# Kernel tuning notes

Hardware: AMD Instinct MI355X
Metric: run time of the kernel (lower is better)

The kernel has to match this reference:

```python
import jax, jax.numpy as jnp
import numpy as np

N_NODES = 100000
N_EDGES = 1600000
GENE_DIM = 256
HID = 128
NUM_CLASSES = 2
BN_EPS = 1e-5


def setup_inputs() -> dict:
    key = jax.random.key(0)
    ks = jax.random.split(key, 24)
    g = lambda k, shape, scale: (jax.random.normal(k, shape, dtype=jnp.float32) * scale)
    inp = {
        "x": g(ks[0], (N_NODES, GENE_DIM), 1.0),
        "edge_index": jax.random.randint(ks[1], (2, N_EDGES), 0, N_NODES, dtype=jnp.int64),
        # GCNConv weights (glorot-ish scale) and biases
        "W1": g(ks[2], (GENE_DIM, HID), 1.0 / np.sqrt(GENE_DIM)), "b1": jnp.zeros((HID,), jnp.float32),
        "W2": g(ks[3], (HID, 2 * HID), 1.0 / np.sqrt(HID)), "b2": jnp.zeros((2 * HID,), jnp.float32),
        "W3": g(ks[4], (2 * HID, HID), 1.0 / np.sqrt(2 * HID)), "b3": jnp.zeros((HID,), jnp.float32),
        "W4": g(ks[5], (HID, HID // 2), 1.0 / np.sqrt(HID)), "b4": jnp.zeros((HID // 2,), jnp.float32),
        "Wc": g(ks[6], (HID // 2, NUM_CLASSES), 1.0 / np.sqrt(HID // 2)), "bc": jnp.zeros((NUM_CLASSES,), jnp.float32),
        # BatchNorm affine params
        "g1": jnp.ones((HID,), jnp.float32), "be1": jnp.zeros((HID,), jnp.float32),
        "g2": jnp.ones((2 * HID,), jnp.float32), "be2": jnp.zeros((2 * HID,), jnp.float32),
        "g3": jnp.ones((HID,), jnp.float32), "be3": jnp.zeros((HID,), jnp.float32),
        "g4": jnp.ones((HID // 2,), jnp.float32), "be4": jnp.zeros((HID // 2,), jnp.float32),
    }
    return inp


def _batchnorm(h, gamma, beta):
    # training-mode BatchNorm1d: per-feature batch stats (biased variance)
    mean = h.mean(axis=0)
    var = ((h - mean) ** 2).mean(axis=0)
    return gamma * (h - mean) * jax.lax.rsqrt(var + BN_EPS) + beta


def _gcn_conv(h, W, b, src, dst, norm, n):
    # PyG GCNConv: linear transform, then sym-normalized aggregation over
    # edges (self-loops already included in src/dst/norm), then bias.
    m = h @ W                                   # [n, d_out]
    msg = m[src] * norm[:, None]                # [E+n, d_out] gather
    agg = jax.ops.segment_sum(msg, dst, num_segments=n)  # scatter-add
    return agg + b


def reference(x, edge_index, W1, b1, W2, b2, W3, b3, W4, b4, Wc, bc,
              g1, be1, g2, be2, g3, be3, g4, be4):
    n = x.shape[0]
    loop = jnp.arange(n, dtype=edge_index.dtype)
    src = jnp.concatenate([edge_index[0], loop])  # add self-loops
    dst = jnp.concatenate([edge_index[1], loop])
    deg = jax.ops.segment_sum(jnp.ones_like(dst, dtype=x.dtype), dst, num_segments=n)
    dinv = jax.lax.rsqrt(jnp.maximum(deg, 1.0))
    norm = dinv[src] * dinv[dst]                  # D^-1/2 (A+I) D^-1/2

    h = jax.nn.relu(_gcn_conv(x, W1, b1, src, dst, norm, n))
    h = _batchnorm(h, g1, be1)
    h = jax.nn.relu(_gcn_conv(h, W2, b2, src, dst, norm, n))
    h = _batchnorm(h, g2, be2)
    h = jax.nn.relu(_gcn_conv(h, W3, b3, src, dst, norm, n))
    h = _batchnorm(h, g3, be3)
    out4 = jax.nn.relu(_gcn_conv(h, W4, b4, src, dst, norm, n))
    bn4 = _batchnorm(out4, g4, be4)
    logits = bn4 @ Wc + bc
    return (logits, out4, bn4)
```

## Files before the change

### kernel.cpp

```cpp
#include <hip/hip_runtime.h>
#include <hip/hip_bf16.h>

#define N_NODES 100000
#define N_EDGES 1600000
#define NB ((N_NODES + 255) / 256)
#define CHUNK 16384
#define NBLK ((N_EDGES + CHUNK - 1) / CHUNK)
#define NSHADOW 64

typedef short sh8 __attribute__((ext_vector_type(8)));
typedef float f32x4 __attribute__((ext_vector_type(4)));

__device__ __forceinline__ float bf2f(unsigned short s) {
    return __uint_as_float(((unsigned int)s) << 16);
}
__device__ __forceinline__ unsigned short f2bf(float f) {
    unsigned int u = __float_as_uint(f);
    unsigned int r = (u + 0x7FFFu + ((u >> 16) & 1u)) >> 16;
    return (unsigned short)r;
}
__device__ __forceinline__ float blo(unsigned int u) { return __uint_as_float(u << 16); }
__device__ __forceinline__ float bhi(unsigned int u) { return __uint_as_float(u & 0xffff0000u); }


__global__ __launch_bounds__(256) void k_hist(const int* __restrict__ ei, int* __restrict__ histG) {
    __shared__ int hist[NB];
    int blk = blockIdx.x, t = threadIdx.x;
    for (int b = t; b < NB; b += 256) hist[b] = 0;
    __syncthreads();
    int e0 = blk * CHUNK;
    int e1 = min(e0 + CHUNK, N_EDGES);
    for (int e = e0 + t; e < e1; e += 256) atomicAdd(&hist[ei[N_EDGES + e] >> 8], 1);
    __syncthreads();
    for (int b = t; b < NB; b += 256) histG[b * NBLK + blk] = hist[b];
}

__global__ __launch_bounds__(128) void k_scanrow(int* __restrict__ histG, int* __restrict__ rowsum) {
    __shared__ int sm[128];
    int b = blockIdx.x, t = threadIdx.x;
    int v = (t < NBLK) ? histG[b * NBLK + t] : 0;
    sm[t] = v; __syncthreads();
    for (int d = 1; d < 128; d <<= 1) {
        int add = (t >= d) ? sm[t - d] : 0;
        __syncthreads(); sm[t] += add; __syncthreads();
    }
    if (t < NBLK) histG[b * NBLK + t] = sm[t] - v;
    if (t == 127) rowsum[b] = sm[127];
}

__global__ __launch_bounds__(512) void k_scanbkt(const int* __restrict__ rowsum, int* __restrict__ rowbase) {
    __shared__ int sm[512];
    int t = threadIdx.x;
    int v = (t < NB) ? rowsum[t] : 0;
    sm[t] = v; __syncthreads();
    for (int d = 1; d < 512; d <<= 1) {
        int add = (t >= d) ? sm[t - d] : 0;
        __syncthreads(); sm[t] += add; __syncthreads();
    }
    if (t <= NB) rowbase[t] = sm[t] - v;
}

__global__ __launch_bounds__(256) void k_part(const int* __restrict__ ei, const int* __restrict__ histG,
                                              const int* __restrict__ rowbase, unsigned* __restrict__ pairs) {
    __shared__ int cur[NB];
    int blk = blockIdx.x, t = threadIdx.x;
    for (int b = t; b < NB; b += 256) cur[b] = rowbase[b] + histG[b * NBLK + blk];
    __syncthreads();
    int e0 = blk * CHUNK;
    int e1 = min(e0 + CHUNK, N_EDGES);
    for (int e = e0 + t; e < e1; e += 256) {
        int s = ei[e], d = ei[N_EDGES + e];
        int pos = atomicAdd(&cur[d >> 8], 1);
        pairs[pos] = ((unsigned)s << 8) | (unsigned)(d & 255);
    }
}

__global__ __launch_bounds__(256) void k_bsort(const unsigned* __restrict__ pairs, const int* __restrict__ rowbase,
                                               int* __restrict__ col, int* __restrict__ basep,
                                               int* __restrict__ deg, float* __restrict__ dinv,
                                               float* __restrict__ sdeg) {
    __shared__ int cnt[256];
    __shared__ int sm[256];
    __shared__ int cur[256];
    int b = blockIdx.x, t = threadIdx.x;
    int base = rowbase[b], end = rowbase[b + 1];
    cnt[t] = 0; __syncthreads();
    for (int e = base + t; e < end; e += 256) atomicAdd(&cnt[pairs[e] & 255], 1);
    __syncthreads();
    int v = cnt[t];
    sm[t] = v; __syncthreads();
    for (int d = 1; d < 256; d <<= 1) {
        int add = (t >= d) ? sm[t - d] : 0;
        __syncthreads(); sm[t] += add; __syncthreads();
    }
    int excl = sm[t] - v;
    cur[t] = excl;
    int gd = (b << 8) + t;
    if (gd < N_NODES) {
        basep[gd] = base + excl;
        deg[gd] = v;
        dinv[gd] = rsqrtf((float)(v + 1));
        sdeg[gd] = sqrtf((float)(v + 1));
    }
    __syncthreads();
    for (int e = base + t; e < end; e += 256) {
        unsigned p = pairs[e];
        int pos = atomicAdd(&cur[p & 255], 1);
        col[base + pos] = (int)(p >> 8);
    }
}

__global__ __launch_bounds__(256) void k_svec(const int* __restrict__ col, const int* __restrict__ basep,
                                              const int* __restrict__ deg, const float* __restrict__ dinv,
                                              float* __restrict__ svec) {
    int w = (blockIdx.x * 256 + threadIdx.x) >> 6;
    if (w >= N_NODES) return;
    int lane = threadIdx.x & 63;
    int start = basep[w], cnt = deg[w];
    float s = 0.f;
    for (int j = lane; j < cnt; j += 64) s += dinv[col[start + j]];
#pragma unroll
    for (int off = 32; off; off >>= 1) s += __shfl_down(s, off, 64);
    if (lane == 0) { float di = dinv[w]; svec[w] = di * (s + di); }
}


__global__ void k_wconv_all(const float* __restrict__ W1, const float* __restrict__ W2,
                            const float* __restrict__ W3, const float* __restrict__ W4,
                            unsigned short* __restrict__ Wt1, unsigned short* __restrict__ Wt2,
                            unsigned short* __restrict__ Wt3, unsigned short* __restrict__ Wt4) {
    int idx = blockIdx.x * 256 + threadIdx.x;
    const float* W; unsigned short* Wt; int K, N, base;
    if (idx < 32768)       { W = W1; Wt = Wt1; K = 256; N = 128; base = 0; }
    else if (idx < 65536)  { W = W2; Wt = Wt2; K = 128; N = 256; base = 32768; }
    else if (idx < 98304)  { W = W3; Wt = Wt3; K = 256; N = 128; base = 65536; }
    else if (idx < 106496) { W = W4; Wt = Wt4; K = 128; N = 64;  base = 98304; }
    else return;
    int li = idx - base;
    int n = li / K, k = li - n * K;
    Wt[li] = f2bf(W[(size_t)k * N + n]);
}


__global__ __launch_bounds__(256) void k_bnred(float* __restrict__ shadow, float* __restrict__ dst) {
    int f = blockIdx.x * 256 + threadIdx.x;
    float s = 0.f;
#pragma unroll
    for (int i = 0; i < NSHADOW; ++i) {
        s += shadow[i * 512 + f];
        shadow[i * 512 + f] = 0.f;
    }
    dst[f] = s;
}


template <int D, bool INF32, bool RESCALE>
__global__ __launch_bounds__(256) void k_bnstats(const void* __restrict__ h,
                                                 const float* __restrict__ sdeg,
                                                 float* __restrict__ shadow) {
    constexpr int VEC = INF32 ? 4 : 8;
    constexpr int TPR = D / VEC;
    constexpr int RPB = 256 / TPR;
    const int tid = threadIdx.x;
    const int rg = tid / TPR;
    const int oc = tid % TPR;
    const int fb = oc * VEC;

    float s1[VEC], s2[VEC];
#pragma unroll
    for (int k = 0; k < VEC; ++k) { s1[k] = 0.f; s2[k] = 0.f; }

    for (int r = blockIdx.x * RPB + rg; r < N_NODES; r += gridDim.x * RPB) {
        float rs = 1.f;
        if constexpr (RESCALE) rs = sdeg[r];
        if constexpr (INF32) {
            float4 v = *(const float4*)((const float*)h + (size_t)r * D + fb);
            float vv[4] = {v.x, v.y, v.z, v.w};
#pragma unroll
            for (int k = 0; k < 4; ++k) {
                float val = vv[k];
                if constexpr (RESCALE) val *= rs;
                s1[k] += val; s2[k] += val * val;
            }
        } else {
            uint4 u = *(const uint4*)((const unsigned short*)h + (size_t)r * D + fb);
            unsigned uu[4] = {u.x, u.y, u.z, u.w};
#pragma unroll
            for (int k = 0; k < 4; ++k) {
                float v0 = blo(uu[k]), v1 = bhi(uu[k]);
                if constexpr (RESCALE) { v0 *= rs; v1 *= rs; }
                s1[2 * k] += v0;     s2[2 * k] += v0 * v0;
                s1[2 * k + 1] += v1; s2[2 * k + 1] += v1 * v1;
            }
        }
    }

    __shared__ float red[2][D];
    for (int i = tid; i < 2 * D; i += 256) ((float*)red)[i] = 0.f;
    __syncthreads();
#pragma unroll
    for (int k = 0; k < VEC; ++k) {
        atomicAdd(&red[0][fb + k], s1[k]);
        atomicAdd(&red[1][fb + k], s2[k]);
    }
    __syncthreads();
    float* slot = shadow + ((blockIdx.x & (NSHADOW - 1)) << 9);
    for (int i = tid; i < 2 * D; i += 256) {
        int f = (i < D) ? i : (256 + i - D);
        float v = (i < D) ? red[0][i] : red[1][i - D];
        atomicAdd(&slot[f], v);
    }
}


template <int BN, int NWM, int NWN, int AMODE, bool BIASRELU, bool DSCALE, bool STATS>
__global__ __launch_bounds__(256) void k_gemm_bf(const void* __restrict__ Ain,
                                                 const unsigned short* __restrict__ Wt,
                                                 const float* __restrict__ sums_in,
                                                 const float* __restrict__ gamma,
                                                 const float* __restrict__ beta,
                                                 const float* __restrict__ svec,
                                                 const float* __restrict__ bias,
                                                 const float* __restrict__ dinv,
                                                 unsigned short* __restrict__ Mout,
                                                 float* __restrict__ sums_out,
                                                 int K, int NTOT) {
    constexpr int BK = 64;
    constexpr int LDA = BK + 8;
    constexpr int MF = 128 / (16 * NWM);
    constexpr int NF = BN / (16 * NWN);
    __shared__ unsigned short As[128 * LDA];
    __shared__ unsigned short Bs[BN * LDA];
    __shared__ float ss_sc[256];
    __shared__ float ss_sh[256];
    const int tid = threadIdx.x;
    const int lane = tid & 63;
    const int w = tid >> 6;
    const int wm = w / NWN, wn = w % NWN;
    const int row0 = blockIdx.x * 128;
    const int col0 = blockIdx.y * BN;

    if constexpr (AMODE >= 1) {
        for (int f = tid; f < K; f += 256) {
            float mean = sums_in[f] * (1.f / N_NODES);
            float var = sums_in[256 + f] * (1.f / N_NODES) - mean * mean;
            float inv = rsqrtf(var + 1e-5f);
            float sc = gamma[f] * inv;
            ss_sc[f] = sc;
            ss_sh[f] = beta[f] - mean * sc;
        }
        __syncthreads();
    }

    f32x4 acc[MF][NF];
#pragma unroll
    for (int i = 0; i < MF; ++i)
#pragma unroll
        for (int j = 0; j < NF; ++j)
#pragma unroll
            for (int r = 0; r < 4; ++r) acc[i][j][r] = 0.f;

    const int sr = tid >> 3;
    const int scc = (tid & 7) * 8;

    for (int k0 = 0; k0 < K; k0 += BK) {
#pragma unroll
        for (int p = 0; p < 4; ++p) {
            int r = p * 32 + sr;
            int gr = row0 + r;
            alignas(16) unsigned short tmp[8];
            if constexpr (AMODE == 0) {
                const float* Af = (const float*)Ain;
                float4 v0 = make_float4(0.f, 0.f, 0.f, 0.f), v1 = v0;
                if (gr < N_NODES) {
                    const float* p0 = Af + (size_t)gr * K + k0 + scc;
                    v0 = *(const float4*)p0;
                    v1 = *(const float4*)(p0 + 4);
                }
                tmp[0] = f2bf(v0.x); tmp[1] = f2bf(v0.y); tmp[2] = f2bf(v0.z); tmp[3] = f2bf(v0.w);
                tmp[4] = f2bf(v1.x); tmp[5] = f2bf(v1.y); tmp[6] = f2bf(v1.z); tmp[7] = f2bf(v1.w);
            } else {
                const unsigned short* Ab = (const unsigned short*)Ain;
                uint4 raw = make_uint4(0, 0, 0, 0);
                if (gr < N_NODES) raw = *(const uint4*)(Ab + (size_t)gr * K + k0 + scc);
                const unsigned short* pr = (const unsigned short*)&raw;
                float sv = 1.f;
                if constexpr (AMODE == 2) sv = (gr < N_NODES) ? svec[gr] : 0.f;
#pragma unroll
                for (int q = 0; q < 8; ++q) {
                    float sc = ss_sc[k0 + scc + q];
                    float sh = ss_sh[k0 + scc + q];
                    float val;
                    if constexpr (AMODE == 2) val = bf2f(pr[q]) * sc + sh * sv;
                    else val = bf2f(pr[q]) * sc + sh;
                    tmp[q] = f2bf(val);
                }
            }
            *(uint4*)&As[r * LDA + scc] = *(const uint4*)tmp;
        }
        constexpr int BP = (BN * BK) / 2048;
#pragma unroll
        for (int p = 0; p < BP; ++p) {
            int r = p * 32 + sr;
            uint4 raw = *(const uint4*)(Wt + (size_t)(col0 + r) * K + k0 + scc);
            *(uint4*)&Bs[r * LDA + scc] = raw;
        }
        __syncthreads();
#pragma unroll
        for (int ks = 0; ks < 2; ++ks) {
            sh8 af[MF], bfr[NF];
#pragma unroll
            for (int i = 0; i < MF; ++i)
                af[i] = *(const sh8*)&As[(wm * MF * 16 + i * 16 + (lane & 15)) * LDA + ks * 32 + (lane >> 4) * 8];
#pragma unroll
            for (int j = 0; j < NF; ++j)
                bfr[j] = *(const sh8*)&Bs[(wn * NF * 16 + j * 16 + (lane & 15)) * LDA + ks * 32 + (lane >> 4) * 8];
#pragma unroll
            for (int i = 0; i < MF; ++i)
#pragma unroll
                for (int j = 0; j < NF; ++j)
                    acc[i][j] = __builtin_amdgcn_mfma_f32_16x16x32_bf16(af[i], bfr[j], acc[i][j], 0, 0, 0);
        }
        __syncthreads();
    }

    float cs[NF], cs2[NF];
    if constexpr (STATS) {
#pragma unroll
        for (int j = 0; j < NF; ++j) { cs[j] = 0.f; cs2[j] = 0.f; }
    }
#pragma unroll
    for (int i = 0; i < MF; ++i) {
#pragma unroll
        for (int r = 0; r < 4; ++r) {
            int grow = row0 + wm * MF * 16 + i * 16 + (lane >> 4) * 4 + r;
            if (grow >= N_NODES) continue;
            float rsc = 1.f;
            if constexpr (DSCALE) rsc = dinv[grow];
#pragma unroll
            for (int j = 0; j < NF; ++j) {
                int gcol = col0 + wn * NF * 16 + j * 16 + (lane & 15);
                float v = acc[i][j][r];
                if constexpr (BIASRELU) v = fmaxf(v + bias[gcol], 0.f);
                if constexpr (DSCALE) v *= rsc;
                if constexpr (STATS) { cs[j] += v; cs2[j] += v * v; }
                Mout[(size_t)grow * NTOT + gcol] = f2bf(v);
            }
        }
    }
    if constexpr (STATS) {
        __shared__ float red[2][BN];
        for (int i = tid; i < 2 * BN; i += 256) ((float*)red)[i] = 0.f;
        __syncthreads();
#pragma unroll
        for (int j = 0; j < NF; ++j) {
            int lc = wn * NF * 16 + j * 16 + (lane & 15);
            atomicAdd(&red[0][lc], cs[j]);
            atomicAdd(&red[1][lc], cs2[j]);
        }
        __syncthreads();
        for (int f = tid; f < BN; f += 256) {
            atomicAdd(&sums_out[col0 + f], red[0][f]);
            atomicAdd(&sums_out[256 + col0 + f], red[1][f]);
        }
    }
}


template <int D, bool PRE, bool OUTF32, bool OUTSCALE>
__global__ __launch_bounds__(256) void k_agg(const unsigned short* __restrict__ m,
                                             const int* __restrict__ col,
                                             const int* __restrict__ basep,
                                             const int* __restrict__ deg,
                                             const float* __restrict__ dinv,
                                             const float* __restrict__ bias,
                                             void* __restrict__ out) {
    constexpr int VPL = D / 64;
    const int w = (blockIdx.x * 256 + threadIdx.x) >> 6;
    if (w >= N_NODES) return;
    const int lane = threadIdx.x & 63;
    const int fo = lane * VPL;
    const unsigned short* mfo = m + fo;
    float acc[VPL];
#pragma unroll
    for (int k = 0; k < VPL; ++k) acc[k] = 0.f;

    int start = basep[w], cnt = deg[w];
    int j = 0;
    for (; j + 8 <= cnt; j += 8) {
        int sx[8];
#pragma unroll
        for (int i = 0; i < 8; ++i) sx[i] = col[start + j + i];
        if constexpr (VPL == 2) {
            unsigned u[8];
#pragma unroll
            for (int i = 0; i < 8; ++i) u[i] = *(const unsigned*)(mfo + (size_t)sx[i] * D);
#pragma unroll
            for (int i = 0; i < 8; ++i) { acc[0] += blo(u[i]); acc[1] += bhi(u[i]); }
        } else {
            float v[8];
#pragma unroll
            for (int i = 0; i < 8; ++i) v[i] = bf2f(mfo[(size_t)sx[i] * D]);
#pragma unroll
            for (int i = 0; i < 8; ++i) acc[0] += v[i];
        }
    }
    for (; j < cnt; ++j) {
        int s0 = col[start + j];
        if constexpr (VPL == 2) {
            unsigned u0 = *(const unsigned*)(mfo + (size_t)s0 * D);
            acc[0] += blo(u0); acc[1] += bhi(u0);
        } else {
            acc[0] += bf2f(mfo[(size_t)s0 * D]);
        }
    }
    if constexpr (VPL == 2) {
        unsigned u0 = *(const unsigned*)(mfo + (size_t)w * D);
        acc[0] += blo(u0); acc[1] += bhi(u0);
    } else {
        acc[0] += bf2f(mfo[(size_t)w * D]);
    }

    float di = dinv[w];
    float o[VPL];
    if constexpr (PRE) {
#pragma unroll
        for (int k = 0; k < VPL; ++k) o[k] = acc[k] * di;
    } else {
#pragma unroll
        for (int k = 0; k < VPL; ++k) {
            o[k] = fmaxf(acc[k] * di + bias[fo + k], 0.f);
            if constexpr (OUTSCALE) o[k] *= di;
        }
    }

    if constexpr (OUTF32) {
        float* of = (float*)out;
#pragma unroll
        for (int k = 0; k < VPL; ++k) of[(size_t)w * D + fo + k] = o[k];
    } else {
        unsigned short* ob = (unsigned short*)out + (size_t)w * D + fo;
        if constexpr (VPL == 2) {
            unsigned int u = (unsigned)f2bf(o[0]) | ((unsigned)f2bf(o[1]) << 16);
            *(unsigned int*)ob = u;
        } else {
            ob[0] = f2bf(o[0]);
        }
    }
}


__global__ __launch_bounds__(256) void k_bnlog(const float* __restrict__ out4, const float* __restrict__ sums,
                                               const float* __restrict__ gamma, const float* __restrict__ beta,
                                               const float* __restrict__ Wc, const float* __restrict__ bc,
                                               float* __restrict__ bn4, float* __restrict__ logits) {
    int gw = (blockIdx.x * 256 + threadIdx.x) >> 6;
    if (gw >= N_NODES) return;
    int f = threadIdx.x & 63;
    float mean = sums[f] * (1.f / N_NODES);
    float var = sums[256 + f] * (1.f / N_NODES) - mean * mean;
    float inv = rsqrtf(var + 1e-5f);
    float sc = gamma[f] * inv;
    float sh = beta[f] - mean * sc;
    float v = out4[(size_t)gw * 64 + f];
    float bn = v * sc + sh;
    bn4[(size_t)gw * 64 + f] = bn;
    float a0 = bn * Wc[2 * f];
    float a1 = bn * Wc[2 * f + 1];
#pragma unroll
    for (int off = 32; off; off >>= 1) {
        a0 += __shfl_down(a0, off, 64);
        a1 += __shfl_down(a1, off, 64);
    }
    if (f == 0) {
        logits[2 * gw] = a0 + bc[0];
        logits[2 * gw + 1] = a1 + bc[1];
    }
}


extern "C" void kernel_launch(void* const* d_in, const int* in_sizes, int n_in,
                              void* d_out, int out_size, void* d_ws, size_t ws_size,
                              hipStream_t stream) {
    const float* x  = (const float*)d_in[0];
    const int* ei   = (const int*)d_in[1];
    const float* W1 = (const float*)d_in[2];  const float* b1  = (const float*)d_in[3];
    const float* W2 = (const float*)d_in[4];  const float* b2  = (const float*)d_in[5];
    const float* W3 = (const float*)d_in[6];  const float* b3  = (const float*)d_in[7];
    const float* W4 = (const float*)d_in[8];  const float* b4  = (const float*)d_in[9];
    const float* Wc = (const float*)d_in[10]; const float* bc  = (const float*)d_in[11];
    const float* g1 = (const float*)d_in[12]; const float* be1 = (const float*)d_in[13];
    const float* g2 = (const float*)d_in[14]; const float* be2 = (const float*)d_in[15];
    const float* g3 = (const float*)d_in[16]; const float* be3 = (const float*)d_in[17];
    const float* g4 = (const float*)d_in[18]; const float* be4 = (const float*)d_in[19];

    char* wsb = (char*)d_ws;
    size_t off = 0;
    auto alloc = [&](size_t bytes) -> void* {
        void* p = wsb + off;
        off = (off + bytes + 511) & ~(size_t)511;
        return p;
    };
    int* deg     = (int*)alloc((size_t)N_NODES * 4);
    int* basep   = (int*)alloc((size_t)N_NODES * 4);
    float* dinv  = (float*)alloc((size_t)N_NODES * 4);
    float* sdeg  = (float*)alloc((size_t)N_NODES * 4);
    float* svec  = (float*)alloc((size_t)N_NODES * 4);
    int* col     = (int*)alloc((size_t)N_EDGES * 4);
    unsigned* pairs = (unsigned*)alloc((size_t)N_EDGES * 4);
    int* histG   = (int*)alloc((size_t)NB * NBLK * 4);
    int* rowsum  = (int*)alloc((size_t)NB * 4);
    int* rowbase = (int*)alloc((size_t)(NB + 1) * 4);
    float* sums  = (float*)alloc(2048 * 4);
    float* shadow = (float*)alloc((size_t)NSHADOW * 512 * 4);
    unsigned short* Wt1 = (unsigned short*)alloc((size_t)256 * 128 * 2);
    unsigned short* Wt2 = (unsigned short*)alloc((size_t)128 * 256 * 2);
    unsigned short* Wt3 = (unsigned short*)alloc((size_t)256 * 128 * 2);
    unsigned short* Wt4 = (unsigned short*)alloc((size_t)128 * 64 * 2);
    unsigned short* mb = (unsigned short*)alloc((size_t)N_NODES * 128 * 2);
    unsigned short* hb = (unsigned short*)alloc((size_t)N_NODES * 256 * 2);

    float* sums1 = sums, *sums2 = sums + 512, *sums3 = sums + 1024, *sums4 = sums + 1536;

    float* outLogits = (float*)d_out;
    float* out4 = outLogits + (size_t)N_NODES * 2;
    float* bn4  = out4 + (size_t)N_NODES * 64;

    hipMemsetAsync(sums, 0, 2048 * 4, stream);
    hipMemsetAsync(shadow, 0, (size_t)NSHADOW * 512 * 4, stream);

    k_hist<<<NBLK, 256, 0, stream>>>(ei, histG);
    k_scanrow<<<NB, 128, 0, stream>>>(histG, rowsum);
    k_scanbkt<<<1, 512, 0, stream>>>(rowsum, rowbase);
    k_part<<<NBLK, 256, 0, stream>>>(ei, histG, rowbase, pairs);
    k_bsort<<<NB, 256, 0, stream>>>(pairs, rowbase, col, basep, deg, dinv, sdeg);
    k_svec<<<(N_NODES + 3) / 4, 256, 0, stream>>>(col, basep, deg, dinv, svec);

    k_wconv_all<<<(106496 + 255) / 256, 256, 0, stream>>>(W1, W2, W3, W4, Wt1, Wt2, Wt3, Wt4);

    const int GBM = (N_NODES + 127) / 128;
    const int AB = (N_NODES + 3) / 4;
    const int SB = 512;

    k_gemm_bf<128, 2, 2, 0, false, true, false><<<dim3(GBM, 1), 256, 0, stream>>>(
        x, Wt1, nullptr, nullptr, nullptr, nullptr, nullptr, dinv, mb, nullptr, 256, 128);
    k_agg<128, false, false, true><<<AB, 256, 0, stream>>>(
        mb, col, basep, deg, dinv, b1, hb);
    k_bnstats<128, false, true><<<SB, 256, 0, stream>>>(hb, sdeg, shadow);
    k_bnred<<<2, 256, 0, stream>>>(shadow, sums1);

    k_agg<128, true, false, false><<<AB, 256, 0, stream>>>(
        hb, col, basep, deg, dinv, nullptr, mb);
    k_gemm_bf<128, 2, 2, 2, true, false, true><<<dim3(GBM, 2), 256, 0, stream>>>(
        mb, Wt2, sums1, g1, be1, svec, b2, nullptr, hb, sums2, 128, 256);

    k_gemm_bf<128, 2, 2, 1, false, true, false><<<dim3(GBM, 1), 256, 0, stream>>>(
        hb, Wt3, sums2, g2, be2, nullptr, nullptr, dinv, mb, nullptr, 256, 128);
    k_agg<128, false, false, false><<<AB, 256, 0, stream>>>(
        mb, col, basep, deg, dinv, b3, hb);
    k_bnstats<128, false, false><<<SB, 256, 0, stream>>>(hb, nullptr, shadow);
    k_bnred<<<2, 256, 0, stream>>>(shadow, sums3);

    k_gemm_bf<64, 4, 1, 1, false, true, false><<<dim3(GBM, 1), 256, 0, stream>>>(
        hb, Wt4, sums3, g3, be3, nullptr, nullptr, dinv, mb, nullptr, 128, 64);
    k_agg<64, false, true, false><<<AB, 256, 0, stream>>>(
        mb, col, basep, deg, dinv, b4, out4);
    k_bnstats<64, true, false><<<SB, 256, 0, stream>>>(out4, nullptr, shadow);
    k_bnred<<<2, 256, 0, stream>>>(shadow, sums4);
    k_bnlog<<<(N_NODES * 64 + 255) / 256, 256, 0, stream>>>(out4, sums4, g4, be4, Wc, bc, bn4, outLogits);
}
```

Before: 629.6 us.

## Register-prefetch GEMM tiles, halve row tile, move layer-2 BN stats to separate kernel

Replaces the bf16 MFMA GEMM with a version that loads the next K-tile from global memory into registers while the current tile is being multiplied, then writes it to LDS afterwards. The row tile drops from 128 to 64 to launch more blocks, and the warp layouts change. BatchNorm statistics are no longer fused into the layer-2 GEMM epilogue; a separate k_bnstats/k_bnred pass over the 256-wide output computes them instead. That extra pass adds a full read of the activation, and the prefetch registers add register pressure.

```diff
diff --git a/kernel.cpp b/kernel.cpp
--- a/kernel.cpp
+++ b/kernel.cpp
@@ -213,23 +213,23 @@
 }
 
 
-template <int BN, int NWM, int NWN, int AMODE, bool BIASRELU, bool DSCALE, bool STATS>
-__global__ __launch_bounds__(256) void k_gemm_bf(const void* __restrict__ Ain,
-                                                 const unsigned short* __restrict__ Wt,
-                                                 const float* __restrict__ sums_in,
-                                                 const float* __restrict__ gamma,
-                                                 const float* __restrict__ beta,
-                                                 const float* __restrict__ svec,
-                                                 const float* __restrict__ bias,
-                                                 const float* __restrict__ dinv,
-                                                 unsigned short* __restrict__ Mout,
-                                                 float* __restrict__ sums_out,
-                                                 int K, int NTOT) {
+template <int BN, int NWM, int NWN, int AMODE, bool BIASRELU, bool DSCALE>
+__global__ __launch_bounds__(256) void k_gemm2(const void* __restrict__ Ain,
+                                               const unsigned short* __restrict__ Wt,
+                                               const float* __restrict__ sums_in,
+                                               const float* __restrict__ gamma,
+                                               const float* __restrict__ beta,
+                                               const float* __restrict__ svec,
+                                               const float* __restrict__ bias,
+                                               const float* __restrict__ dinv,
+                                               unsigned short* __restrict__ Mout,
+                                               int K, int NTOT) {
     constexpr int BK = 64;
-    constexpr int LDA = BK + 8;
-    constexpr int MF = 128 / (16 * NWM);
+    constexpr int LDA = 72;
+    constexpr int MF = 64 / (16 * NWM);
     constexpr int NF = BN / (16 * NWN);
-    __shared__ unsigned short As[128 * LDA];
+    constexpr int BP = BN / 32;
+    __shared__ unsigned short As[64 * LDA];
     __shared__ unsigned short Bs[BN * LDA];
     __shared__ float ss_sc[256];
     __shared__ float ss_sh[256];
@@ -237,7 +237,7 @@
     const int lane = tid & 63;
     const int w = tid >> 6;
     const int wm = w / NWN, wn = w % NWN;
-    const int row0 = blockIdx.x * 128;
+    const int row0 = blockIdx.x * 64;
     const int col0 = blockIdx.y * BN;
 
     if constexpr (AMODE >= 1) {
@@ -252,60 +252,85 @@
         __syncthreads();
     }
 
-    f32x4 acc[MF][NF];
-#pragma unroll
-    for (int i = 0; i < MF; ++i)
-#pragma unroll
-        for (int j = 0; j < NF; ++j)
-#pragma unroll
-            for (int r = 0; r < 4; ++r) acc[i][j][r] = 0.f;
-
     const int sr = tid >> 3;
     const int scc = (tid & 7) * 8;
 
-    for (int k0 = 0; k0 < K; k0 += BK) {
-#pragma unroll
-        for (int p = 0; p < 4; ++p) {
+    float4 fa[2][2];
+    uint4 ua[2];
+    uint4 ub[BP];
+    float sv[2];
+
+    auto LOAD = [&](int k0) {
+        if constexpr (AMODE == 0) {
+            const float* Af = (const float*)Ain;
+#pragma unroll
+            for (int p = 0; p < 2; ++p) {
+                int gr = row0 + p * 32 + sr;
+                fa[p][0] = make_float4(0.f, 0.f, 0.f, 0.f); fa[p][1] = fa[p][0];
+                if (gr < N_NODES) {
+                    const float* p0 = Af + (size_t)gr * K + k0 + scc;
+                    fa[p][0] = *(const float4*)p0;
+                    fa[p][1] = *(const float4*)(p0 + 4);
+                }
+            }
+        } else {
+            const unsigned short* Ab = (const unsigned short*)Ain;
+#pragma unroll
+            for (int p = 0; p < 2; ++p) {
+                int gr = row0 + p * 32 + sr;
+                ua[p] = make_uint4(0, 0, 0, 0);
+                if (gr < N_NODES) ua[p] = *(const uint4*)(Ab + (size_t)gr * K + k0 + scc);
+                if constexpr (AMODE == 2) sv[p] = (gr < N_NODES) ? svec[gr] : 0.f;
+            }
+        }
+#pragma unroll
+        for (int p = 0; p < BP; ++p) {
             int r = p * 32 + sr;
-            int gr = row0 + r;
+            ub[p] = *(const uint4*)(Wt + (size_t)(col0 + r) * K + k0 + scc);
+        }
+    };
+
+    auto WRITE = [&](int k0) {
+#pragma unroll
+        for (int p = 0; p < 2; ++p) {
             alignas(16) unsigned short tmp[8];
             if constexpr (AMODE == 0) {
-                const float* Af = (const float*)Ain;
-                float4 v0 = make_float4(0.f, 0.f, 0.f, 0.f), v1 = v0;
-                if (gr < N_NODES) {
-                    const float* p0 = Af + (size_t)gr * K + k0 + scc;
-                    v0 = *(const float4*)p0;
-                    v1 = *(const float4*)(p0 + 4);
-                }
-                tmp[0] = f2bf(v0.x); tmp[1] = f2bf(v0.y); tmp[2] = f2bf(v0.z); tmp[3] = f2bf(v0.w);
-                tmp[4] = f2bf(v1.x); tmp[5] = f2bf(v1.y); tmp[6] = f2bf(v1.z); tmp[7] = f2bf(v1.w);
+                tmp[0] = f2bf(fa[p][0].x); tmp[1] = f2bf(fa[p][0].y);
+                tmp[2] = f2bf(fa[p][0].z); tmp[3] = f2bf(fa[p][0].w);
+                tmp[4] = f2bf(fa[p][1].x); tmp[5] = f2bf(fa[p][1].y);
+                tmp[6] = f2bf(fa[p][1].z); tmp[7] = f2bf(fa[p][1].w);
             } else {
-                const unsigned short* Ab = (const unsigned short*)Ain;
-                uint4 raw = make_uint4(0, 0, 0, 0);
-                if (gr < N_NODES) raw = *(const uint4*)(Ab + (size_t)gr * K + k0 + scc);
-                const unsigned short* pr = (const unsigned short*)&raw;
-                float sv = 1.f;
-                if constexpr (AMODE == 2) sv = (gr < N_NODES) ? svec[gr] : 0.f;
+                const unsigned short* pr = (const unsigned short*)&ua[p];
 #pragma unroll
                 for (int q = 0; q < 8; ++q) {
                     float sc = ss_sc[k0 + scc + q];
                     float sh = ss_sh[k0 + scc + q];
                     float val;
-                    if constexpr (AMODE == 2) val = bf2f(pr[q]) * sc + sh * sv;
+                    if constexpr (AMODE == 2) val = bf2f(pr[q]) * sc + sh * sv[p];
                     else val = bf2f(pr[q]) * sc + sh;
                     tmp[q] = f2bf(val);
                 }
             }
-            *(uint4*)&As[r * LDA + scc] = *(const uint4*)tmp;
-        }
-        constexpr int BP = (BN * BK) / 2048;
-#pragma unroll
-        for (int p = 0; p < BP; ++p) {
-            int r = p * 32 + sr;
-            uint4 raw = *(const uint4*)(Wt + (size_t)(col0 + r) * K + k0 + scc);
-            *(uint4*)&Bs[r * LDA + scc] = raw;
-        }
-        __syncthreads();
+            *(uint4*)&As[(p * 32 + sr) * LDA + scc] = *(const uint4*)tmp;
+        }
+#pragma unroll
+        for (int p = 0; p < BP; ++p) *(uint4*)&Bs[(p * 32 + sr) * LDA + scc] = ub[p];
+    };
+
+    f32x4 acc[MF][NF];
+#pragma unroll
+    for (int i = 0; i < MF; ++i)
+#pragma unroll
+        for (int j = 0; j < NF; ++j)
+#pragma unroll
+            for (int r = 0; r < 4; ++r) acc[i][j][r] = 0.f;
+
+    LOAD(0);
+    WRITE(0);
+    __syncthreads();
+    const int nk = K / BK;
+    for (int kt = 1; kt <= nk; ++kt) {
+        if (kt < nk) LOAD(kt * BK);
 #pragma unroll
         for (int ks = 0; ks < 2; ++ks) {
             sh8 af[MF], bfr[NF];
@@ -322,13 +347,12 @@
                     acc[i][j] = __builtin_amdgcn_mfma_f32_16x16x32_bf16(af[i], bfr[j], acc[i][j], 0, 0, 0);
         }
         __syncthreads();
-    }
-
-    float cs[NF], cs2[NF];
-    if constexpr (STATS) {
-#pragma unroll
-        for (int j = 0; j < NF; ++j) { cs[j] = 0.f; cs2[j] = 0.f; }
-    }
+        if (kt < nk) {
+            WRITE(kt * BK);
+            __syncthreads();
+        }
+    }
+
 #pragma unroll
     for (int i = 0; i < MF; ++i) {
 #pragma unroll
@@ -343,25 +367,8 @@
                 float v = acc[i][j][r];
                 if constexpr (BIASRELU) v = fmaxf(v + bias[gcol], 0.f);
                 if constexpr (DSCALE) v *= rsc;
-                if constexpr (STATS) { cs[j] += v; cs2[j] += v * v; }
                 Mout[(size_t)grow * NTOT + gcol] = f2bf(v);
             }
-        }
-    }
-    if constexpr (STATS) {
-        __shared__ float red[2][BN];
-        for (int i = tid; i < 2 * BN; i += 256) ((float*)red)[i] = 0.f;
-        __syncthreads();
-#pragma unroll
-        for (int j = 0; j < NF; ++j) {
-            int lc = wn * NF * 16 + j * 16 + (lane & 15);
-            atomicAdd(&red[0][lc], cs[j]);
-            atomicAdd(&red[1][lc], cs2[j]);
-        }
-        __syncthreads();
-        for (int f = tid; f < BN; f += 256) {
-            atomicAdd(&sums_out[col0 + f], red[0][f]);
-            atomicAdd(&sums_out[256 + col0 + f], red[1][f]);
         }
     }
 }
@@ -538,12 +545,12 @@
 
     k_wconv_all<<<(106496 + 255) / 256, 256, 0, stream>>>(W1, W2, W3, W4, Wt1, Wt2, Wt3, Wt4);
 
-    const int GBM = (N_NODES + 127) / 128;
+    const int GBM = (N_NODES + 63) / 64;
     const int AB = (N_NODES + 3) / 4;
     const int SB = 512;
 
-    k_gemm_bf<128, 2, 2, 0, false, true, false><<<dim3(GBM, 1), 256, 0, stream>>>(
-        x, Wt1, nullptr, nullptr, nullptr, nullptr, nullptr, dinv, mb, nullptr, 256, 128);
+    k_gemm2<128, 1, 4, 0, false, true><<<dim3(GBM, 1), 256, 0, stream>>>(
+        x, Wt1, nullptr, nullptr, nullptr, nullptr, nullptr, dinv, mb, 256, 128);
     k_agg<128, false, false, true><<<AB, 256, 0, stream>>>(
         mb, col, basep, deg, dinv, b1, hb);
     k_bnstats<128, false, true><<<SB, 256, 0, stream>>>(hb, sdeg, shadow);
@@ -551,18 +558,20 @@
 
     k_agg<128, true, false, false><<<AB, 256, 0, stream>>>(
         hb, col, basep, deg, dinv, nullptr, mb);
-    k_gemm_bf<128, 2, 2, 2, true, false, true><<<dim3(GBM, 2), 256, 0, stream>>>(
-        mb, Wt2, sums1, g1, be1, svec, b2, nullptr, hb, sums2, 128, 256);
-
-    k_gemm_bf<128, 2, 2, 1, false, true, false><<<dim3(GBM, 1), 256, 0, stream>>>(
-        hb, Wt3, sums2, g2, be2, nullptr, nullptr, dinv, mb, nullptr, 256, 128);
+    k_gemm2<128, 1, 4, 2, true, false><<<dim3(GBM, 2), 256, 0, stream>>>(
+        mb, Wt2, sums1, g1, be1, svec, b2, nullptr, hb, 128, 256);
+    k_bnstats<256, false, false><<<SB, 256, 0, stream>>>(hb, nullptr, shadow);
+    k_bnred<<<2, 256, 0, stream>>>(shadow, sums2);
+
+    k_gemm2<128, 1, 4, 1, false, true><<<dim3(GBM, 1), 256, 0, stream>>>(
+        hb, Wt3, sums2, g2, be2, nullptr, nullptr, dinv, mb, 256, 128);
     k_agg<128, false, false, false><<<AB, 256, 0, stream>>>(
         mb, col, basep, deg, dinv, b3, hb);
     k_bnstats<128, false, false><<<SB, 256, 0, stream>>>(hb, nullptr, shadow);
     k_bnred<<<2, 256, 0, stream>>>(shadow, sums3);
 
-    k_gemm_bf<64, 4, 1, 1, false, true, false><<<dim3(GBM, 1), 256, 0, stream>>>(
-        hb, Wt4, sums3, g3, be3, nullptr, nullptr, dinv, mb, nullptr, 128, 64);
+    k_gemm2<64, 2, 2, 1, false, true><<<dim3(GBM, 1), 256, 0, stream>>>(
+        hb, Wt4, sums3, g3, be3, nullptr, nullptr, dinv, mb, 128, 64);
     k_agg<64, false, true, false><<<AB, 256, 0, stream>>>(
         mb, col, basep, deg, dinv, b4, out4);
     k_bnstats<64, true, false><<<SB, 256, 0, stream>>>(out4, nullptr, shadow);
```

After: 660.4 us. 4.9% more time.
